# Optimization experiments

Hardware: AMD Instinct MI355X
Metric: run time of the kernel (lower is better)

## Reference

```python
import jax, jax.numpy as jnp
import numpy as np


def gcn_layer(x, src, dst, deg_inv_sqrt, W, b):
    # PyG GCNConv: h = X W; out[i] = sum_{j->i} norm(j,i) * h[j] + deg_i^{-1} * h[i] + b
    n = x.shape[0]
    h = x @ W                                   # [N, out]
    norm = deg_inv_sqrt[src] * deg_inv_sqrt[dst]  # [E]
    msg = h[src] * norm[:, None]                # [E, out]
    agg = jax.ops.segment_sum(msg, dst, num_segments=n)
    # self-loop contribution (added loops with norm = deg_i^{-1})
    agg = agg + h * (deg_inv_sqrt * deg_inv_sqrt)[:, None]
    return agg + b


def setup_inputs() -> dict:
    key = jax.random.key(0)
    k1, k2, k3, k4, k5, k6 = jax.random.split(key, 6)
    N, E, IN, HID, OUT = 50000, 800000, 128, 128, 64
    x = jax.random.normal(k1, (N, IN), dtype=jnp.float32)
    edge_index = jax.random.randint(k2, (2, E), 0, N, dtype=jnp.int64)
    # glorot-ish init for weights, zeros-ish bias
    W1 = jax.random.normal(k3, (IN, HID), dtype=jnp.float32) * (1.0 / np.sqrt(IN))
    b1 = jax.random.normal(k4, (HID,), dtype=jnp.float32) * 0.01
    W2 = jax.random.normal(k5, (HID, OUT), dtype=jnp.float32) * (1.0 / np.sqrt(HID))
    b2 = jax.random.normal(k6, (OUT,), dtype=jnp.float32) * 0.01
    return {"x": x, "edge_index": edge_index, "W1": W1, "b1": b1, "W2": W2, "b2": b2}


def reference(x, edge_index, W1, b1, W2, b2):
    n = x.shape[0]
    src, dst = edge_index[0], edge_index[1]
    # degree with self-loops (PyG computes degree on the dst/col index)
    deg = jax.ops.segment_sum(jnp.ones_like(dst, dtype=x.dtype), dst, num_segments=n) + 1.0
    deg_inv_sqrt = jax.lax.rsqrt(deg)
    h = gcn_layer(x, src, dst, deg_inv_sqrt, W1, b1)
    h = jax.nn.relu(h)
    # F.dropout with training=False is identity (module evaluated in eval mode)
    out = gcn_layer(h, src, dst, deg_inv_sqrt, W2, b2)
    return out
```

## Files before the change

### kernel.cpp

```cpp
#include <hip/hip_runtime.h>
#include <stdint.h>

typedef __attribute__((ext_vector_type(8))) short short8;
typedef __attribute__((ext_vector_type(4))) float floatx4;

static inline size_t align256(size_t x) { return (x + 255) & ~size_t(255); }

__device__ __forceinline__ unsigned short f2bf(float f) {
    unsigned u = __float_as_uint(f);
    u += 0x7fff + ((u >> 16) & 1);
    return (unsigned short)(u >> 16);
}
__device__ __forceinline__ unsigned pack_bf16(float a, float b) {
    return (unsigned)f2bf(a) | ((unsigned)f2bf(b) << 16);
}
__device__ __forceinline__ float bf_lo(unsigned u) { return __uint_as_float(u << 16); }
__device__ __forceinline__ float bf_hi(unsigned u) { return __uint_as_float(u & 0xffff0000u); }

#define BSHIFT 7
#define NBMAX 1024
#define CH 2048

__device__ __forceinline__ bool detect_i32(const void* eidx, int E, int t) {
    const long long* e64 = (const long long*)eidx;
    int nchk = E < 256 ? E : 256;
    long long v = e64[t % nchk];
    int bad = (v < 0 || v > 0x7fffffffLL) ? 1 : 0;
    return __syncthreads_or(bad) != 0;
}

__global__ __launch_bounds__(256) void k_hist(const void* __restrict__ eidx, int E,
                                              int* __restrict__ counts,
                                              int* __restrict__ chist, int NB, int NC) {
    __shared__ int hist[NBMAX];
    const int t = threadIdx.x, c = blockIdx.x;
    const int e0 = c * CH;
    const int e1 = (e0 + CH < E) ? e0 + CH : E;
    const bool i32 = detect_i32(eidx, E, t);
    const int* e32 = (const int*)eidx;
    const long long* e64 = (const long long*)eidx;
    for (int b0 = 0; b0 < NB; b0 += NBMAX) {
        int bw = (NB - b0 < NBMAX) ? NB - b0 : NBMAX;
        for (int i = t; i < bw; i += 256) hist[i] = 0;
        __syncthreads();
        for (int e = e0 + t; e < e1; e += 256) {
            int d = i32 ? e32[(size_t)E + e] : (int)e64[(size_t)E + e];
            if (b0 == 0) atomicAdd(&counts[d], 1);
            int b = (d >> BSHIFT) - b0;
            if (b >= 0 && b < bw) atomicAdd(&hist[b], 1);
        }
        __syncthreads();
        for (int i = t; i < bw; i += 256) chist[(size_t)(b0 + i) * NC + c] = hist[i];
        __syncthreads();
    }
}

__global__ __launch_bounds__(1024) void k_scan1(const int* __restrict__ counts,
                                                int* __restrict__ row_start,
                                                int* __restrict__ bsum, int N) {
    __shared__ int swt[16];
    __shared__ int swt2[16];
    const int t = threadIdx.x, lane = t & 63, w = t >> 6;
    int i = blockIdx.x * 1024 + t;
    int v = (i < N) ? counts[i] : 0;
    int incl = v;
    #pragma unroll
    for (int off = 1; off < 64; off <<= 1) {
        int nbr = __shfl_up(incl, off, 64);
        if (lane >= off) incl += nbr;
    }
    if (lane == 63) swt[w] = incl;
    __syncthreads();
    if (w == 0) {
        int wincl = (lane < 16) ? swt[lane] : 0;
        #pragma unroll
        for (int off = 1; off < 16; off <<= 1) {
            int nbr = __shfl_up(wincl, off, 64);
            if (lane >= off) wincl += nbr;
        }
        if (lane < 16) swt2[lane] = wincl;
    }
    __syncthreads();
    int excl = ((w == 0) ? 0 : swt2[w - 1]) + incl - v;
    if (i < N) row_start[i] = excl;
    if (t == 0) bsum[blockIdx.x] = swt2[15];
}

__global__ __launch_bounds__(1024) void k_scan2(const int* __restrict__ bsum,
                                                int* __restrict__ bexc,
                                                int* __restrict__ row_start,
                                                int nblk, int N) {
    __shared__ int swt[16];
    __shared__ int swt2[16];
    const int t = threadIdx.x, lane = t & 63, w = t >> 6;
    int carry = 0;
    for (int base = 0; base < nblk; base += 1024) {
        int i = base + t;
        int v = (i < nblk) ? bsum[i] : 0;
        int incl = v;
        #pragma unroll
        for (int off = 1; off < 64; off <<= 1) {
            int nbr = __shfl_up(incl, off, 64);
            if (lane >= off) incl += nbr;
        }
        if (lane == 63) swt[w] = incl;
        __syncthreads();
        if (w == 0) {
            int wincl = (lane < 16) ? swt[lane] : 0;
            #pragma unroll
            for (int off = 1; off < 16; off <<= 1) {
                int nbr = __shfl_up(wincl, off, 64);
                if (lane >= off) wincl += nbr;
            }
            if (lane < 16) swt2[lane] = wincl;
        }
        __syncthreads();
        int excl = carry + ((w == 0) ? 0 : swt2[w - 1]) + incl - v;
        if (i < nblk) bexc[i] = excl;
        carry += swt2[15];
        __syncthreads();
    }
    if (t == 0) row_start[N] = carry;
}

__global__ void k_scan3(int* __restrict__ row_start, int* __restrict__ pos,
                        const int* __restrict__ bexc, const int* __restrict__ counts,
                        float* __restrict__ dinv, int N) {
    int i = blockIdx.x * blockDim.x + threadIdx.x;
    if (i < N) {
        int r = row_start[i] + bexc[i >> 10];
        row_start[i] = r;
        pos[i] = r;
        dinv[i] = rsqrtf((float)counts[i] + 1.0f);
    }
}

__global__ __launch_bounds__(256) void k_hscan(int* __restrict__ chist,
                                               const int* __restrict__ row_start,
                                               int NB, int NC) {
    int b = blockIdx.x * 4 + (threadIdx.x >> 6);
    if (b >= NB) return;
    int lane = threadIdx.x & 63;
    int* row = chist + (size_t)b * NC;
    int carry = row_start[b << BSHIFT];
    for (int base = 0; base < NC; base += 64) {
        int i = base + lane;
        int v = (i < NC) ? row[i] : 0;
        int incl = v;
        #pragma unroll
        for (int off = 1; off < 64; off <<= 1) {
            int nbr = __shfl_up(incl, off, 64);
            if (lane >= off) incl += nbr;
        }
        if (i < NC) row[i] = carry + incl - v;
        carry += __shfl(incl, 63, 64);
    }
}

__global__ __launch_bounds__(256) void k_bfill(const void* __restrict__ eidx, int E,
                                               const int* __restrict__ chist,
                                               uint2* __restrict__ bbuf, int NB, int NC) {
    __shared__ int rank[NBMAX];
    __shared__ int base[NBMAX];
    const int t = threadIdx.x, c = blockIdx.x;
    const int e0 = c * CH;
    const int e1 = (e0 + CH < E) ? e0 + CH : E;
    const bool i32 = detect_i32(eidx, E, t);
    const int* e32 = (const int*)eidx;
    const long long* e64 = (const long long*)eidx;
    for (int b0 = 0; b0 < NB; b0 += NBMAX) {
        int bw = (NB - b0 < NBMAX) ? NB - b0 : NBMAX;
        for (int i = t; i < bw; i += 256) {
            rank[i] = 0;
            base[i] = chist[(size_t)(b0 + i) * NC + c];
        }
        __syncthreads();
        for (int e = e0 + t; e < e1; e += 256) {
            int s, d;
            if (i32) { s = e32[e]; d = e32[(size_t)E + e]; }
            else     { s = (int)e64[e]; d = (int)e64[(size_t)E + e]; }
            int b = (d >> BSHIFT) - b0;
            if (b >= 0 && b < bw) {
                int slot = base[b] + atomicAdd(&rank[b], 1);
                bbuf[slot] = make_uint2((unsigned)s, (unsigned)d);
            }
        }
        __syncthreads();
    }
}

__global__ void k_fill2(const uint2* __restrict__ bbuf, int E,
                        int* __restrict__ pos, int* __restrict__ esrc) {
    int i = blockIdx.x * blockDim.x + threadIdx.x;
    if (i >= E) return;
    uint2 sd = bbuf[i];
    int p = atomicAdd(&pos[sd.y], 1);
    esrc[p] = (int)sd.x;
}

__global__ void k_cvt(const float* __restrict__ x, unsigned short* __restrict__ xb, int n8,
                      const float* __restrict__ W1, const float* __restrict__ W2,
                      unsigned short* __restrict__ w1t, unsigned short* __restrict__ w2t,
                      int K1, int M1, int K2, int M2) {
    int idx = blockIdx.x * blockDim.x + threadIdx.x;
    if (idx < n8) {
        float4 a = ((const float4*)x)[2 * idx];
        float4 b = ((const float4*)x)[2 * idx + 1];
        uint4 o;
        o.x = pack_bf16(a.x, a.y); o.y = pack_bf16(a.z, a.w);
        o.z = pack_bf16(b.x, b.y); o.w = pack_bf16(b.z, b.w);
        ((uint4*)xb)[idx] = o;
        return;
    }
    int j = idx - n8;
    if (j < K1 * M1) {
        int k = j / M1, n = j % M1;
        w1t[(size_t)n * K1 + k] = f2bf(W1[j]);
    } else if (j - K1 * M1 < K2 * M2) {
        int j2 = j - K1 * M1;
        int k = j2 / M2, n = j2 % M2;
        w2t[(size_t)n * K2 + k] = f2bf(W2[j2]);
    }
}

__global__ __launch_bounds__(256, 4) void k_gemm_mfma(
        const unsigned short* __restrict__ A,
        const unsigned short* __restrict__ Bt,
        const float* __restrict__ dinv,
        unsigned short* __restrict__ C,
        int N, int M) {
    constexpr int LD = 136;
    __shared__ unsigned short As[64 * LD];
    __shared__ unsigned short Bs[64 * LD];
    const int tid = threadIdx.x;
    const int wave = tid >> 6, lane = tid & 63;
    const int q = lane >> 4, tm = lane & 15;
    const int row0 = blockIdx.x * 64;
    const int c0 = blockIdx.y * 64;

    {
        const uint4* Ag = (const uint4*)A;
        const uint4* Bg = (const uint4*)Bt;
        #pragma unroll
        for (int it = 0; it < 4; ++it) {
            int i = tid + it * 256;
            int r = i >> 4, o = i & 15;
            int row = row0 + r;
            uint4 v = make_uint4(0, 0, 0, 0);
            if (row < N) v = Ag[(size_t)row * 16 + o];
            *(uint4*)&As[r * LD + o * 8] = v;
            *(uint4*)&Bs[r * LD + o * 8] = Bg[(size_t)(c0 + r) * 16 + o];
        }
    }
    __syncthreads();

    floatx4 acc[4];
    #pragma unroll
    for (int g = 0; g < 4; ++g) acc[g] = (floatx4){0.f, 0.f, 0.f, 0.f};

    const int arow = wave * 16 + tm;
    #pragma unroll
    for (int kc = 0; kc < 4; ++kc) {
        short8 af = *(const short8*)&As[arow * LD + kc * 32 + q * 8];
        #pragma unroll
        for (int g = 0; g < 4; ++g) {
            short8 bf = *(const short8*)&Bs[(g * 16 + tm) * LD + kc * 32 + q * 8];
            acc[g] = __builtin_amdgcn_mfma_f32_16x16x32_bf16(af, bf, acc[g], 0, 0, 0);
        }
    }

    float dv[4];
    #pragma unroll
    for (int r = 0; r < 4; ++r) {
        int row = row0 + wave * 16 + q * 4 + r;
        dv[r] = (row < N) ? dinv[row] : 0.f;
    }
    #pragma unroll
    for (int g = 0; g < 4; ++g) {
        #pragma unroll
        for (int r = 0; r < 4; ++r) {
            int row = row0 + wave * 16 + q * 4 + r;
            if (row < N) C[(size_t)row * M + c0 + g * 16 + tm] = f2bf(dv[r] * acc[g][r]);
        }
    }
}

__global__ __launch_bounds__(256) void k_agg128(const unsigned* __restrict__ Hb,
        const float* __restrict__ dinv, const int* __restrict__ rs,
        const int* __restrict__ esrc, const float* __restrict__ bias,
        unsigned* __restrict__ out, int N) {
    int wid = (blockIdx.x * 256 + threadIdx.x) >> 6;
    if (wid >= N) return;
    int l = threadIdx.x & 63;
    float di = dinv[wid];
    unsigned a = Hb[(size_t)wid * 64 + l];
    float accx = bf_lo(a), accy = bf_hi(a);
    int k = rs[wid], kend = rs[wid + 1];
    for (; k + 8 <= kend; k += 8) {
        int s[8];
        #pragma unroll
        for (int j = 0; j < 8; ++j) s[j] = esrc[k + j];
        unsigned g[8];
        #pragma unroll
        for (int j = 0; j < 8; ++j) g[j] = Hb[(size_t)s[j] * 64 + l];
        #pragma unroll
        for (int j = 0; j < 8; ++j) { accx += bf_lo(g[j]); accy += bf_hi(g[j]); }
    }
    if (k + 4 <= kend) {
        int s[4];
        #pragma unroll
        for (int j = 0; j < 4; ++j) s[j] = esrc[k + j];
        unsigned g[4];
        #pragma unroll
        for (int j = 0; j < 4; ++j) g[j] = Hb[(size_t)s[j] * 64 + l];
        #pragma unroll
        for (int j = 0; j < 4; ++j) { accx += bf_lo(g[j]); accy += bf_hi(g[j]); }
        k += 4;
    }
    for (; k < kend; ++k) {
        unsigned g = Hb[(size_t)esrc[k] * 64 + l];
        accx += bf_lo(g); accy += bf_hi(g);
    }
    float2 b = ((const float2*)bias)[l];
    float ox = fmaxf(fmaf(di, accx, b.x), 0.f);
    float oy = fmaxf(fmaf(di, accy, b.y), 0.f);
    out[(size_t)wid * 64 + l] = pack_bf16(ox, oy);
}

__global__ __launch_bounds__(256) void k_agg64(const unsigned short* __restrict__ Hb,
        const float* __restrict__ dinv, const int* __restrict__ rs,
        const int* __restrict__ esrc, const float* __restrict__ bias,
        float* __restrict__ out, int N) {
    int wid = (blockIdx.x * 256 + threadIdx.x) >> 6;
    if (wid >= N) return;
    int l = threadIdx.x & 63;
    float di = dinv[wid];
    float acc = __uint_as_float((unsigned)Hb[(size_t)wid * 64 + l] << 16);
    int k = rs[wid], kend = rs[wid + 1];
    for (; k + 8 <= kend; k += 8) {
        int s[8];
        #pragma unroll
        for (int j = 0; j < 8; ++j) s[j] = esrc[k + j];
        unsigned short g[8];
        #pragma unroll
        for (int j = 0; j < 8; ++j) g[j] = Hb[(size_t)s[j] * 64 + l];
        #pragma unroll
        for (int j = 0; j < 8; ++j) acc += __uint_as_float((unsigned)g[j] << 16);
    }
    if (k + 4 <= kend) {
        int s[4];
        #pragma unroll
        for (int j = 0; j < 4; ++j) s[j] = esrc[k + j];
        unsigned short g[4];
        #pragma unroll
        for (int j = 0; j < 4; ++j) g[j] = Hb[(size_t)s[j] * 64 + l];
        #pragma unroll
        for (int j = 0; j < 4; ++j) acc += __uint_as_float((unsigned)g[j] << 16);
        k += 4;
    }
    for (; k < kend; ++k)
        acc += __uint_as_float((unsigned)Hb[(size_t)esrc[k] * 64 + l] << 16);
    out[(size_t)wid * 64 + l] = fmaf(di, acc, bias[l]);
}

extern "C" void kernel_launch(void* const* d_in, const int* in_sizes, int n_in,
                              void* d_out, int out_size, void* d_ws, size_t ws_size,
                              hipStream_t stream) {
    const float* x  = (const float*)d_in[0];
    const void*  ei = d_in[1];
    const float* W1 = (const float*)d_in[2];
    const float* b1 = (const float*)d_in[3];
    const float* W2 = (const float*)d_in[4];
    const float* b2 = (const float*)d_in[5];

    const int HID = in_sizes[3];
    const int IN  = in_sizes[2] / HID;
    const int OUT = in_sizes[4] / HID;
    const int N   = in_sizes[0] / IN;
    const int E   = in_sizes[1] / 2;
    const int NBLK = (N + 1023) / 1024;
    const int NB   = (N + 127) >> BSHIFT;
    const int NC   = (E + CH - 1) / CH;

    char* p = (char*)d_ws;
    int* counts    = (int*)p;   p += align256((size_t)N * 4);
    int* row_start = (int*)p;   p += align256((size_t)(N + 1) * 4);
    int* pos       = (int*)p;   p += align256((size_t)N * 4);
    int* bsum      = (int*)p;   p += align256((size_t)NBLK * 4);
    int* bexc      = (int*)p;   p += align256((size_t)NBLK * 4);
    int* chist     = (int*)p;   p += align256((size_t)NB * NC * 4);
    int* esrc      = (int*)p;   p += align256((size_t)E * 4);
    float* dinv    = (float*)p; p += align256((size_t)N * 4);
    unsigned short* w1t = (unsigned short*)p; p += align256((size_t)HID * IN * 2);
    unsigned short* w2t = (unsigned short*)p; p += align256((size_t)OUT * HID * 2);
    unsigned short* xb  = (unsigned short*)p; p += align256((size_t)N * IN * 2);
    size_t hb_bytes = (size_t)N * HID * 2, bbuf_bytes = (size_t)E * 8;
    uint2* bbuf    = (uint2*)p;
    unsigned short* hb = (unsigned short*)p;
    p += align256(hb_bytes > bbuf_bytes ? hb_bytes : bbuf_bytes);
    unsigned short* h1b = (unsigned short*)p; p += align256((size_t)N * HID * 2);
    unsigned short* h2b = (unsigned short*)p; p += align256((size_t)N * OUT * 2);

    hipMemsetAsync(counts, 0, (size_t)N * 4, stream);

    k_hist<<<NC, 256, 0, stream>>>(ei, E, counts, chist, NB, NC);
    k_scan1<<<NBLK, 1024, 0, stream>>>(counts, row_start, bsum, N);
    k_scan2<<<1, 1024, 0, stream>>>(bsum, bexc, row_start, NBLK, N);
    k_scan3<<<(N + 255) / 256, 256, 0, stream>>>(row_start, pos, bexc, counts, dinv, N);
    k_hscan<<<(NB + 3) / 4, 256, 0, stream>>>(chist, row_start, NB, NC);
    k_bfill<<<NC, 256, 0, stream>>>(ei, E, chist, bbuf, NB, NC);
    k_fill2<<<(E + 255) / 256, 256, 0, stream>>>(bbuf, E, pos, esrc);

    const int n8 = N * IN / 8;
    k_cvt<<<(n8 + IN * HID + HID * OUT + 255) / 256, 256, 0, stream>>>(
        x, xb, n8, W1, W2, w1t, w2t, IN, HID, HID, OUT);

    k_gemm_mfma<<<dim3((N + 63) / 64, HID / 64), 256, 0, stream>>>(xb, w1t, dinv, hb, N, HID);
    k_agg128<<<(N + 3) / 4, 256, 0, stream>>>((unsigned*)hb, dinv, row_start, esrc, b1,
                                              (unsigned*)h1b, N);

    k_gemm_mfma<<<dim3((N + 63) / 64, OUT / 64), 256, 0, stream>>>(h1b, w2t, dinv, h2b, N, OUT);
    k_agg64<<<(N + 3) / 4, 256, 0, stream>>>(h2b, dinv, row_start, esrc, b2, (float*)d_out, N);
}
```

Before: 246.6 us.

## Fuse CSR build into one cooperative kernel and fold x conversion into GEMM

Merges the separate graph-preprocessing steps into one cooperative kernel separated by grid-wide syncs: histogram, the three scan passes, bucket scan, bucket fill, final scatter, and the weight transpose/convert. This removes many small launches and the memset. The first GEMM now reads fp32 x and converts it to bf16 while loading shared memory, which drops the separate conversion pass and the xb buffer. The GEMM is templated so each block computes the full output width, so the weights load once per row tile. Costs: grid.sync overheads, a requirement that every block be co-resident, and a single-block second scan that limits N to 65536 nodes.

After: 516.5 us. 2.09x slower.

```diff
diff --git a/kernel.cpp b/kernel.cpp
--- a/kernel.cpp
+++ b/kernel.cpp
@@ -1,5 +1,8 @@
 #include <hip/hip_runtime.h>
+#include <hip/hip_cooperative_groups.h>
 #include <stdint.h>
+
+namespace cg = cooperative_groups;
 
 typedef __attribute__((ext_vector_type(8))) short short8;
 typedef __attribute__((ext_vector_type(4))) float floatx4;
@@ -29,218 +32,195 @@
     return __syncthreads_or(bad) != 0;
 }
 
-__global__ __launch_bounds__(256) void k_hist(const void* __restrict__ eidx, int E,
-                                              int* __restrict__ counts,
-                                              int* __restrict__ chist, int NB, int NC) {
-    __shared__ int hist[NBMAX];
-    const int t = threadIdx.x, c = blockIdx.x;
-    const int e0 = c * CH;
-    const int e1 = (e0 + CH < E) ? e0 + CH : E;
-    const bool i32 = detect_i32(eidx, E, t);
+__global__ __launch_bounds__(256) void k_csr(
+        const void* __restrict__ eidx, int E, int N,
+        int* __restrict__ counts, int* __restrict__ chist,
+        int* __restrict__ row_start, int* __restrict__ rs_final,
+        int* __restrict__ pos, int* __restrict__ bsum, int* __restrict__ bexc,
+        float* __restrict__ dinv, uint2* __restrict__ bbuf, int* __restrict__ esrc,
+        const float* __restrict__ W1, const float* __restrict__ W2,
+        unsigned short* __restrict__ w1t, unsigned short* __restrict__ w2t,
+        int K1, int M1, int K2, int M2,
+        int NB, int NC, int NS, int NH) {
+    __shared__ int shA[NBMAX];
+    __shared__ int shB[NBMAX];
+    cg::grid_group grid = cg::this_grid();
+    const int t = threadIdx.x, B = blockIdx.x, G = gridDim.x;
+    const int lane = t & 63, w = t >> 6;
     const int* e32 = (const int*)eidx;
     const long long* e64 = (const long long*)eidx;
-    for (int b0 = 0; b0 < NB; b0 += NBMAX) {
-        int bw = (NB - b0 < NBMAX) ? NB - b0 : NBMAX;
-        for (int i = t; i < bw; i += 256) hist[i] = 0;
-        __syncthreads();
-        for (int e = e0 + t; e < e1; e += 256) {
-            int d = i32 ? e32[(size_t)E + e] : (int)e64[(size_t)E + e];
-            if (b0 == 0) atomicAdd(&counts[d], 1);
-            int b = (d >> BSHIFT) - b0;
-            if (b >= 0 && b < bw) atomicAdd(&hist[b], 1);
-        }
-        __syncthreads();
-        for (int i = t; i < bw; i += 256) chist[(size_t)(b0 + i) * NC + c] = hist[i];
-        __syncthreads();
-    }
-}
-
-__global__ __launch_bounds__(1024) void k_scan1(const int* __restrict__ counts,
-                                                int* __restrict__ row_start,
-                                                int* __restrict__ bsum, int N) {
-    __shared__ int swt[16];
-    __shared__ int swt2[16];
-    const int t = threadIdx.x, lane = t & 63, w = t >> 6;
-    int i = blockIdx.x * 1024 + t;
-    int v = (i < N) ? counts[i] : 0;
-    int incl = v;
-    #pragma unroll
-    for (int off = 1; off < 64; off <<= 1) {
-        int nbr = __shfl_up(incl, off, 64);
-        if (lane >= off) incl += nbr;
-    }
-    if (lane == 63) swt[w] = incl;
-    __syncthreads();
-    if (w == 0) {
-        int wincl = (lane < 16) ? swt[lane] : 0;
-        #pragma unroll
-        for (int off = 1; off < 16; off <<= 1) {
-            int nbr = __shfl_up(wincl, off, 64);
-            if (lane >= off) wincl += nbr;
-        }
-        if (lane < 16) swt2[lane] = wincl;
-    }
-    __syncthreads();
-    int excl = ((w == 0) ? 0 : swt2[w - 1]) + incl - v;
-    if (i < N) row_start[i] = excl;
-    if (t == 0) bsum[blockIdx.x] = swt2[15];
-}
-
-__global__ __launch_bounds__(1024) void k_scan2(const int* __restrict__ bsum,
-                                                int* __restrict__ bexc,
-                                                int* __restrict__ row_start,
-                                                int nblk, int N) {
-    __shared__ int swt[16];
-    __shared__ int swt2[16];
-    const int t = threadIdx.x, lane = t & 63, w = t >> 6;
-    int carry = 0;
-    for (int base = 0; base < nblk; base += 1024) {
-        int i = base + t;
-        int v = (i < nblk) ? bsum[i] : 0;
+
+    for (int i = B * 256 + t; i < N; i += G * 256) counts[i] = 0;
+    grid.sync();
+
+    if (B < NC) {
+        const int e0 = B * CH;
+        const int e1 = (e0 + CH < E) ? e0 + CH : E;
+        const bool i32 = detect_i32(eidx, E, t);
+        for (int b0 = 0; b0 < NB; b0 += NBMAX) {
+            int bw = (NB - b0 < NBMAX) ? NB - b0 : NBMAX;
+            for (int i = t; i < bw; i += 256) shA[i] = 0;
+            __syncthreads();
+            for (int e = e0 + t; e < e1; e += 256) {
+                int d = i32 ? e32[(size_t)E + e] : (int)e64[(size_t)E + e];
+                if (b0 == 0) atomicAdd(&counts[d], 1);
+                int b = (d >> BSHIFT) - b0;
+                if (b >= 0 && b < bw) atomicAdd(&shA[b], 1);
+            }
+            __syncthreads();
+            for (int i = t; i < bw; i += 256) chist[(size_t)(b0 + i) * NC + B] = shA[i];
+            __syncthreads();
+        }
+    } else if (B == NC) {
+        for (int j = t; j < K1 * M1; j += 256) {
+            int k = j / M1, n = j % M1;
+            w1t[(size_t)n * K1 + k] = f2bf(W1[j]);
+        }
+    } else if (B == NC + 1) {
+        for (int j = t; j < K2 * M2; j += 256) {
+            int k = j / M2, n = j % M2;
+            w2t[(size_t)n * K2 + k] = f2bf(W2[j]);
+        }
+    }
+    grid.sync();
+
+    if (B < NS) {
+        int i = B * 256 + t;
+        int v = (i < N) ? counts[i] : 0;
         int incl = v;
         #pragma unroll
         for (int off = 1; off < 64; off <<= 1) {
             int nbr = __shfl_up(incl, off, 64);
             if (lane >= off) incl += nbr;
         }
-        if (lane == 63) swt[w] = incl;
+        if (lane == 63) shA[w] = incl;
         __syncthreads();
-        if (w == 0) {
-            int wincl = (lane < 16) ? swt[lane] : 0;
-            #pragma unroll
-            for (int off = 1; off < 16; off <<= 1) {
-                int nbr = __shfl_up(wincl, off, 64);
-                if (lane >= off) wincl += nbr;
-            }
-            if (lane < 16) swt2[lane] = wincl;
-        }
-        __syncthreads();
-        int excl = carry + ((w == 0) ? 0 : swt2[w - 1]) + incl - v;
-        if (i < nblk) bexc[i] = excl;
-        carry += swt2[15];
-        __syncthreads();
-    }
-    if (t == 0) row_start[N] = carry;
-}
-
-__global__ void k_scan3(int* __restrict__ row_start, int* __restrict__ pos,
-                        const int* __restrict__ bexc, const int* __restrict__ counts,
-                        float* __restrict__ dinv, int N) {
-    int i = blockIdx.x * blockDim.x + threadIdx.x;
-    if (i < N) {
-        int r = row_start[i] + bexc[i >> 10];
-        row_start[i] = r;
-        pos[i] = r;
-        dinv[i] = rsqrtf((float)counts[i] + 1.0f);
-    }
-}
-
-__global__ __launch_bounds__(256) void k_hscan(int* __restrict__ chist,
-                                               const int* __restrict__ row_start,
-                                               int NB, int NC) {
-    int b = blockIdx.x * 4 + (threadIdx.x >> 6);
-    if (b >= NB) return;
-    int lane = threadIdx.x & 63;
-    int* row = chist + (size_t)b * NC;
-    int carry = row_start[b << BSHIFT];
-    for (int base = 0; base < NC; base += 64) {
-        int i = base + lane;
-        int v = (i < NC) ? row[i] : 0;
+        int woff = 0;
+        for (int j = 0; j < w; ++j) woff += shA[j];
+        if (i < N) row_start[i] = woff + incl - v;
+        if (t == 255) bsum[B] = woff + incl;
+    }
+    grid.sync();
+
+    if (B == 0) {
+        int v = (t < NS) ? bsum[t] : 0;
         int incl = v;
         #pragma unroll
         for (int off = 1; off < 64; off <<= 1) {
             int nbr = __shfl_up(incl, off, 64);
             if (lane >= off) incl += nbr;
         }
-        if (i < NC) row[i] = carry + incl - v;
-        carry += __shfl(incl, 63, 64);
-    }
-}
-
-__global__ __launch_bounds__(256) void k_bfill(const void* __restrict__ eidx, int E,
-                                               const int* __restrict__ chist,
-                                               uint2* __restrict__ bbuf, int NB, int NC) {
-    __shared__ int rank[NBMAX];
-    __shared__ int base[NBMAX];
-    const int t = threadIdx.x, c = blockIdx.x;
-    const int e0 = c * CH;
-    const int e1 = (e0 + CH < E) ? e0 + CH : E;
-    const bool i32 = detect_i32(eidx, E, t);
-    const int* e32 = (const int*)eidx;
-    const long long* e64 = (const long long*)eidx;
-    for (int b0 = 0; b0 < NB; b0 += NBMAX) {
-        int bw = (NB - b0 < NBMAX) ? NB - b0 : NBMAX;
-        for (int i = t; i < bw; i += 256) {
-            rank[i] = 0;
-            base[i] = chist[(size_t)(b0 + i) * NC + c];
-        }
+        if (lane == 63) shA[w] = incl;
         __syncthreads();
-        for (int e = e0 + t; e < e1; e += 256) {
-            int s, d;
-            if (i32) { s = e32[e]; d = e32[(size_t)E + e]; }
-            else     { s = (int)e64[e]; d = (int)e64[(size_t)E + e]; }
-            int b = (d >> BSHIFT) - b0;
-            if (b >= 0 && b < bw) {
-                int slot = base[b] + atomicAdd(&rank[b], 1);
-                bbuf[slot] = make_uint2((unsigned)s, (unsigned)d);
+        int woff = 0;
+        for (int j = 0; j < w; ++j) woff += shA[j];
+        if (t < NS) bexc[t] = woff + incl - v;
+        if (t == 255) row_start[N] = woff + incl;
+    }
+    grid.sync();
+
+    if (B < NS) {
+        int i = B * 256 + t;
+        if (i < N) {
+            int r = row_start[i] + bexc[B];
+            rs_final[i] = r;
+            pos[i] = r;
+            dinv[i] = rsqrtf((float)counts[i] + 1.0f);
+        }
+        if (B == 0 && t == 0) rs_final[N] = row_start[N];
+    } else if (B < NS + NH) {
+        int b = (B - NS) * 4 + w;
+        if (b < NB) {
+            int node = b << BSHIFT;
+            int* row = chist + (size_t)b * NC;
+            int carry = row_start[node] + bexc[node >> 8];
+            for (int base = 0; base < NC; base += 64) {
+                int i = base + lane;
+                int v = (i < NC) ? row[i] : 0;
+                int incl = v;
+                #pragma unroll
+                for (int off = 1; off < 64; off <<= 1) {
+                    int nbr = __shfl_up(incl, off, 64);
+                    if (lane >= off) incl += nbr;
+                }
+                if (i < NC) row[i] = carry + incl - v;
+                carry += __shfl(incl, 63, 64);
             }
         }
-        __syncthreads();
-    }
-}
-
-__global__ void k_fill2(const uint2* __restrict__ bbuf, int E,
-                        int* __restrict__ pos, int* __restrict__ esrc) {
-    int i = blockIdx.x * blockDim.x + threadIdx.x;
-    if (i >= E) return;
-    uint2 sd = bbuf[i];
-    int p = atomicAdd(&pos[sd.y], 1);
-    esrc[p] = (int)sd.x;
-}
-
-__global__ void k_cvt(const float* __restrict__ x, unsigned short* __restrict__ xb, int n8,
-                      const float* __restrict__ W1, const float* __restrict__ W2,
-                      unsigned short* __restrict__ w1t, unsigned short* __restrict__ w2t,
-                      int K1, int M1, int K2, int M2) {
-    int idx = blockIdx.x * blockDim.x + threadIdx.x;
-    if (idx < n8) {
-        float4 a = ((const float4*)x)[2 * idx];
-        float4 b = ((const float4*)x)[2 * idx + 1];
-        uint4 o;
-        o.x = pack_bf16(a.x, a.y); o.y = pack_bf16(a.z, a.w);
-        o.z = pack_bf16(b.x, b.y); o.w = pack_bf16(b.z, b.w);
-        ((uint4*)xb)[idx] = o;
-        return;
-    }
-    int j = idx - n8;
-    if (j < K1 * M1) {
-        int k = j / M1, n = j % M1;
-        w1t[(size_t)n * K1 + k] = f2bf(W1[j]);
-    } else if (j - K1 * M1 < K2 * M2) {
-        int j2 = j - K1 * M1;
-        int k = j2 / M2, n = j2 % M2;
-        w2t[(size_t)n * K2 + k] = f2bf(W2[j2]);
-    }
-}
-
-__global__ __launch_bounds__(256, 4) void k_gemm_mfma(
-        const unsigned short* __restrict__ A,
-        const unsigned short* __restrict__ Bt,
-        const float* __restrict__ dinv,
-        unsigned short* __restrict__ C,
+    }
+    grid.sync();
+
+    if (B < NC) {
+        const int e0 = B * CH;
+        const int e1 = (e0 + CH < E) ? e0 + CH : E;
+        const bool i32 = detect_i32(eidx, E, t);
+        for (int b0 = 0; b0 < NB; b0 += NBMAX) {
+            int bw = (NB - b0 < NBMAX) ? NB - b0 : NBMAX;
+            for (int i = t; i < bw; i += 256) {
+                shA[i] = 0;
+                shB[i] = chist[(size_t)(b0 + i) * NC + B];
+            }
+            __syncthreads();
+            for (int e = e0 + t; e < e1; e += 256) {
+                int s, d;
+                if (i32) { s = e32[e]; d = e32[(size_t)E + e]; }
+                else     { s = (int)e64[e]; d = (int)e64[(size_t)E + e]; }
+                int b = (d >> BSHIFT) - b0;
+                if (b >= 0 && b < bw) {
+                    int slot = shB[b] + atomicAdd(&shA[b], 1);
+                    bbuf[slot] = make_uint2((unsigned)s, (unsigned)d);
+                }
+            }
+            __syncthreads();
+        }
+    }
+    grid.sync();
+
+    for (int i = B * 256 + t; i < E; i += G * 256) {
+        uint2 sd = bbuf[i];
+        int p = atomicAdd(&pos[sd.y], 1);
+        esrc[p] = (int)sd.x;
+    }
+}
+
+template<int BN, bool AF32>
+__global__ __launch_bounds__(256, 3) void k_gemm(
+        const void* __restrict__ Av, const unsigned short* __restrict__ Bt,
+        const float* __restrict__ dinv, unsigned short* __restrict__ C,
         int N, int M) {
     constexpr int LD = 136;
     __shared__ unsigned short As[64 * LD];
-    __shared__ unsigned short Bs[64 * LD];
+    __shared__ unsigned short Bs[BN * LD];
     const int tid = threadIdx.x;
     const int wave = tid >> 6, lane = tid & 63;
     const int q = lane >> 4, tm = lane & 15;
     const int row0 = blockIdx.x * 64;
-    const int c0 = blockIdx.y * 64;
 
     {
-        const uint4* Ag = (const uint4*)A;
         const uint4* Bg = (const uint4*)Bt;
+        #pragma unroll
+        for (int it = 0; it < BN / 16; ++it) {
+            int i = tid + it * 256;
+            int r = i >> 4, o = i & 15;
+            *(uint4*)&Bs[r * LD + o * 8] = Bg[(size_t)r * 16 + o];
+        }
+    }
+    if (AF32) {
+        const float4* Ag = (const float4*)Av;
+        #pragma unroll
+        for (int it = 0; it < 8; ++it) {
+            int i = tid + it * 256;
+            int r = i >> 5, o = i & 31;
+            int row = row0 + r;
+            float4 v = make_float4(0.f, 0.f, 0.f, 0.f);
+            if (row < N) v = Ag[(size_t)row * 32 + o];
+            uint2 pk;
+            pk.x = pack_bf16(v.x, v.y);
+            pk.y = pack_bf16(v.z, v.w);
+            *(uint2*)&As[r * LD + o * 4] = pk;
+        }
+    } else {
+        const uint4* Ag = (const uint4*)Av;
         #pragma unroll
         for (int it = 0; it < 4; ++it) {
             int i = tid + it * 256;
@@ -249,21 +229,21 @@
             uint4 v = make_uint4(0, 0, 0, 0);
             if (row < N) v = Ag[(size_t)row * 16 + o];
             *(uint4*)&As[r * LD + o * 8] = v;
-            *(uint4*)&Bs[r * LD + o * 8] = Bg[(size_t)(c0 + r) * 16 + o];
         }
     }
     __syncthreads();
 
-    floatx4 acc[4];
+    constexpr int NG = BN / 16;
+    floatx4 acc[NG];
     #pragma unroll
-    for (int g = 0; g < 4; ++g) acc[g] = (floatx4){0.f, 0.f, 0.f, 0.f};
+    for (int g = 0; g < NG; ++g) acc[g] = (floatx4){0.f, 0.f, 0.f, 0.f};
 
     const int arow = wave * 16 + tm;
     #pragma unroll
     for (int kc = 0; kc < 4; ++kc) {
         short8 af = *(const short8*)&As[arow * LD + kc * 32 + q * 8];
         #pragma unroll
-        for (int g = 0; g < 4; ++g) {
+        for (int g = 0; g < NG; ++g) {
             short8 bf = *(const short8*)&Bs[(g * 16 + tm) * LD + kc * 32 + q * 8];
             acc[g] = __builtin_amdgcn_mfma_f32_16x16x32_bf16(af, bf, acc[g], 0, 0, 0);
         }
@@ -276,11 +256,11 @@
         dv[r] = (row < N) ? dinv[row] : 0.f;
     }
     #pragma unroll
-    for (int g = 0; g < 4; ++g) {
+    for (int g = 0; g < NG; ++g) {
         #pragma unroll
         for (int r = 0; r < 4; ++r) {
             int row = row0 + wave * 16 + q * 4 + r;
-            if (row < N) C[(size_t)row * M + c0 + g * 16 + tm] = f2bf(dv[r] * acc[g][r]);
+            if (row < N) C[(size_t)row * M + g * 16 + tm] = f2bf(dv[r] * acc[g][r]);
         }
     }
 }
@@ -373,27 +353,28 @@
     const float* W2 = (const float*)d_in[4];
     const float* b2 = (const float*)d_in[5];
 
-    const int HID = in_sizes[3];
-    const int IN  = in_sizes[2] / HID;
-    const int OUT = in_sizes[4] / HID;
-    const int N   = in_sizes[0] / IN;
-    const int E   = in_sizes[1] / 2;
-    const int NBLK = (N + 1023) / 1024;
-    const int NB   = (N + 127) >> BSHIFT;
-    const int NC   = (E + CH - 1) / CH;
+    int HID = in_sizes[3];
+    int IN  = in_sizes[2] / HID;
+    int OUT = in_sizes[4] / HID;
+    int N   = in_sizes[0] / IN;
+    int E   = in_sizes[1] / 2;
+    int NB  = (N + 127) >> BSHIFT;
+    int NC  = (E + CH - 1) / CH;
+    int NS  = (N + 255) / 256;
+    int NH  = (NB + 3) / 4;
 
     char* p = (char*)d_ws;
     int* counts    = (int*)p;   p += align256((size_t)N * 4);
     int* row_start = (int*)p;   p += align256((size_t)(N + 1) * 4);
+    int* rs_final  = (int*)p;   p += align256((size_t)(N + 1) * 4);
     int* pos       = (int*)p;   p += align256((size_t)N * 4);
-    int* bsum      = (int*)p;   p += align256((size_t)NBLK * 4);
-    int* bexc      = (int*)p;   p += align256((size_t)NBLK * 4);
+    int* bsum      = (int*)p;   p += align256((size_t)NS * 4);
+    int* bexc      = (int*)p;   p += align256((size_t)NS * 4);
     int* chist     = (int*)p;   p += align256((size_t)NB * NC * 4);
     int* esrc      = (int*)p;   p += align256((size_t)E * 4);
     float* dinv    = (float*)p; p += align256((size_t)N * 4);
     unsigned short* w1t = (unsigned short*)p; p += align256((size_t)HID * IN * 2);
     unsigned short* w2t = (unsigned short*)p; p += align256((size_t)OUT * HID * 2);
-    unsigned short* xb  = (unsigned short*)p; p += align256((size_t)N * IN * 2);
     size_t hb_bytes = (size_t)N * HID * 2, bbuf_bytes = (size_t)E * 8;
     uint2* bbuf    = (uint2*)p;
     unsigned short* hb = (unsigned short*)p;
@@ -401,24 +382,23 @@
     unsigned short* h1b = (unsigned short*)p; p += align256((size_t)N * HID * 2);
     unsigned short* h2b = (unsigned short*)p; p += align256((size_t)N * OUT * 2);
 
-    hipMemsetAsync(counts, 0, (size_t)N * 4, stream);
-
-    k_hist<<<NC, 256, 0, stream>>>(ei, E, counts, chist, NB, NC);
-    k_scan1<<<NBLK, 1024, 0, stream>>>(counts, row_start, bsum, N);
-    k_scan2<<<1, 1024, 0, stream>>>(bsum, bexc, row_start, NBLK, N);
-    k_scan3<<<(N + 255) / 256, 256, 0, stream>>>(row_start, pos, bexc, counts, dinv, N);
-    k_hscan<<<(NB + 3) / 4, 256, 0, stream>>>(chist, row_start, NB, NC);
-    k_bfill<<<NC, 256, 0, stream>>>(ei, E, chist, bbuf, NB, NC);
-    k_fill2<<<(E + 255) / 256, 256, 0, stream>>>(bbuf, E, pos, esrc);
-
-    const int n8 = N * IN / 8;
-    k_cvt<<<(n8 + IN * HID + HID * OUT + 255) / 256, 256, 0, stream>>>(
-        x, xb, n8, W1, W2, w1t, w2t, IN, HID, HID, OUT);
-
-    k_gemm_mfma<<<dim3((N + 63) / 64, HID / 64), 256, 0, stream>>>(xb, w1t, dinv, hb, N, HID);
-    k_agg128<<<(N + 3) / 4, 256, 0, stream>>>((unsigned*)hb, dinv, row_start, esrc, b1,
+    int G = NC + 2;
+    if (G < NS + NH) G = NS + NH;
+    void* args[] = {
+        (void*)&ei, (void*)&E, (void*)&N,
+        (void*)&counts, (void*)&chist, (void*)&row_start, (void*)&rs_final,
+        (void*)&pos, (void*)&bsum, (void*)&bexc, (void*)&dinv,
+        (void*)&bbuf, (void*)&esrc,
+        (void*)&W1, (void*)&W2, (void*)&w1t, (void*)&w2t,
+        (void*)&IN, (void*)&HID, (void*)&HID, (void*)&OUT,
+        (void*)&NB, (void*)&NC, (void*)&NS, (void*)&NH,
+    };
+    hipLaunchCooperativeKernel((void*)k_csr, dim3(G), dim3(256), args, 0, stream);
+
+    k_gemm<128, true><<<(N + 63) / 64, 256, 0, stream>>>(x, w1t, dinv, hb, N, HID);
+    k_agg128<<<(N + 3) / 4, 256, 0, stream>>>((unsigned*)hb, dinv, rs_final, esrc, b1,
                                               (unsigned*)h1b, N);
 
-    k_gemm_mfma<<<dim3((N + 63) / 64, OUT / 64), 256, 0, stream>>>(h1b, w2t, dinv, h2b, N, OUT);
-    k_agg64<<<(N + 3) / 4, 256, 0, stream>>>(h2b, dinv, row_start, esrc, b2, (float*)d_out, N);
-}
+    k_gemm<64, false><<<(N + 63) / 64, 256, 0, stream>>>(h1b, w2t, dinv, h2b, N, OUT);
+    k_agg64<<<(N + 3) / 4, 256, 0, stream>>>(h2b, dinv, rs_final, esrc, b2, (float*)d_out, N);
+}
```
